# Optimization experiments

Measured on AMD Instinct MI355X. Metric: run time of the kernel, lower is better.

## Reference

```python
import jax, jax.numpy as jnp
import numpy as np
import math, itertools

NUM_FEATURES = 128
NUM_ELEMENTS = 10
BATCH = 2048
LS_IN = [0, 1, 2]            # coupling irreps 0e+1o+2e (parity = (-1)^l)
BLOCKS = [(0, 1), (1, -1)]   # output irreps 0e, 1o as (L, parity)
CORRELATION = 3


def _su2_cg(j1, m1, j2, m2, j3, m3):
    if m3 != m1 + m2 or not (abs(j1 - j2) <= j3 <= j1 + j2):
        return 0.0
    f = math.factorial
    pref = math.sqrt((2 * j3 + 1) * f(j3 + j1 - j2) * f(j3 - j1 + j2) * f(j1 + j2 - j3) / f(j1 + j2 + j3 + 1))
    pref *= math.sqrt(f(j3 + m3) * f(j3 - m3) * f(j1 - m1) * f(j1 + m1) * f(j2 - m2) * f(j2 + m2))
    s = 0.0
    for k in range(max(0, j2 - j3 - m1, j1 - j3 + m2), min(j1 + j2 - j3, j1 - m1, j2 + m2) + 1):
        s += (-1) ** k / (f(k) * f(j1 + j2 - j3 - k) * f(j1 - m1 - k) * f(j2 + m2 - k) * f(j3 - j2 + m1 + k) * f(j3 - j1 - m2 + k))
    return pref * s


def _c2r(l):
    # complex -> real spherical harmonic change of basis (unitary)
    Q = np.zeros((2 * l + 1, 2 * l + 1), dtype=complex)
    Q[l, l] = 1.0
    for m in range(1, l + 1):
        Q[l + m, l + m] = (-1) ** m / math.sqrt(2)
        Q[l + m, l - m] = 1 / math.sqrt(2)
        Q[l - m, l - m] = 1j / math.sqrt(2)
        Q[l - m, l + m] = -1j * (-1) ** m / math.sqrt(2)
    return Q


def _real_cg(l1, l2, l3):
    C = np.zeros((2 * l1 + 1, 2 * l2 + 1, 2 * l3 + 1), dtype=complex)
    for m1 in range(-l1, l1 + 1):
        for m2 in range(-l2, l2 + 1):
            m3 = m1 + m2
            if abs(m3) <= l3:
                C[l1 + m1, l2 + m2, l3 + m3] = _su2_cg(l1, m1, l2, m2, l3, m3)
    T = np.einsum('am,bn,co,mno->abc', _c2r(l1).conj(), _c2r(l2).conj(), _c2r(l3), C)
    if np.abs(T.imag).max() > np.abs(T.real).max():
        T = 1j * T  # tensor is purely real or purely imaginary depending on l1+l2+l3
    return np.ascontiguousarray(T.real)


def _build_paths(segs, num_ell, nu):
    # left-to-right CG coupling of nu copies of the input coupling irreps
    cur = {}
    for l, off in segs:
        T = np.zeros((2 * l + 1, num_ell))
        for m in range(2 * l + 1):
            T[m, off + m] = 1.0
        cur.setdefault((l, (-1) ** l), []).append(T)
    for _ in range(nu - 1):
        nxt = {}
        for (la, pa), ts in cur.items():
            for lb, off in segs:
                for lc in range(abs(la - lb), la + lb + 1):
                    C = _real_cg(la, lb, lc)
                    for T in ts:
                        M = np.einsum('abc,a...->c...b', C, T)
                        new = np.zeros(M.shape[:-1] + (num_ell,))
                        new[..., off:off + 2 * lb + 1] = M
                        nxt.setdefault((lc, pa * (-1) ** lb), []).append(new)
        cur = nxt
    return cur


def _u_matrix(segs, num_ell, nu, L, parity):
    # symmetrized, orthonormalized generalized CG basis: (2L+1, num_ell^nu..., P)
    ts = _build_paths(segs, num_ell, nu).get((L, parity), [])
    dimL = 2 * L + 1
    perms = list(itertools.permutations(range(nu)))
    mats = []
    for T in ts:
        S = sum(np.transpose(T, (0,) + tuple(1 + p for p in perm)) for perm in perms) / len(perms)
        mats.append(S.reshape(-1))
    if not mats:
        return np.zeros((dimL,) + (num_ell,) * nu + (0,))
    _, s, Vh = np.linalg.svd(np.stack(mats), full_matrices=False)
    B = Vh[s > 1e-9 * s[0]]
    return np.moveaxis(B.reshape((-1, dimL) + (num_ell,) * nu), 0, -1)


def setup_inputs() -> dict:
    key = jax.random.key(0)
    kx, ky, kw = jax.random.split(key, 3)
    num_ell = sum(2 * l + 1 for l in LS_IN)  # 9
    segs, off = [], 0
    for l in LS_IN:
        segs.append((l, off))
        off += 2 * l + 1
    x = jax.random.normal(kx, (BATCH, NUM_FEATURES, num_ell), dtype=jnp.float32)
    elem = jax.random.randint(ky, (BATCH,), 0, NUM_ELEMENTS)
    y = jax.nn.one_hot(elem, NUM_ELEMENTS, dtype=jnp.float32)  # one-hot element types
    inp = {"x": x, "y": y}
    for bi, (L, par) in enumerate(BLOCKS):
        Us = {nu: _u_matrix(segs, num_ell, nu, L, par) for nu in range(1, CORRELATION + 1)}
        std = 1.0 / max(sum(U.shape[-1] for U in Us.values()), 1)  # RandomNormal(1/total_params)
        for nu, U in Us.items():
            kw, sub = jax.random.split(kw)
            inp[f"U{nu}_{bi}"] = jnp.asarray(U, dtype=jnp.float32)
            inp[f"W{nu}_{bi}"] = std * jax.random.normal(sub, (NUM_ELEMENTS, U.shape[-1], NUM_FEATURES), dtype=jnp.float32)
    return inp


def _block(x, y, U3, U2, U1, W3, W2, W1):
    # x: (B,C,n), y: (B,E); U_nu: (D, n^nu..., P_nu); W_nu: (E, P_nu, C)
    # degree-3 term: fuse per-element weights and x into the last ell axis of U3
    w3 = jnp.einsum('be,epc->bcp', y, W3)            # (B,C,P3)
    z = x[:, :, :, None] * w3[:, :, None, :]         # (B,C,n,P3)
    out = jnp.einsum('dijkp,bckp->bcdij', U3, z)     # (B,C,D,n,n)
    # degree-2 term added, then contract one more ell axis with x
    c2 = jnp.einsum('dijp,bpc->bcdij', U2, jnp.einsum('be,epc->bpc', y, W2)) + out
    out = jnp.einsum('bcdij,bcj->bcdi', c2, x)
    # degree-1 term added, final contraction
    c1 = jnp.einsum('dip,bpc->bcdi', U1, jnp.einsum('be,epc->bpc', y, W1)) + out
    out = jnp.einsum('bcdi,bci->bcd', c1, x)
    B, C, D = out.shape
    return out.reshape(B, C * D)  # mul_ir (mul-major) layout


def reference(x, y, U1_0, U2_0, U3_0, W1_0, W2_0, W3_0, U1_1, U2_1, U3_1, W1_1, W2_1, W3_1):
    o0 = _block(x, y, U3_0, U2_0, U1_0, W3_0, W2_0, W1_0)  # 128x0e block
    o1 = _block(x, y, U3_1, U2_1, U1_1, W3_1, W2_1, W1_1)  # 128x1o block
    return jnp.concatenate([o0, o1], axis=-1)
```

## Files before the change

kernel.cpp:

```cpp
#include <hip/hip_runtime.h>

#define NELL 9
#define CCH  128
#define DB   3
#define P3A  5
#define P2A  3
#define P1A  1
#define P3B  5
#define P2B  2
#define P1B  1
#define NT3  165
#define NT2  45
#define TTOT (NT3 + NT2 + NELL)
#define CPB  8
#define NCG  (CCH / CPB)
#define CHR  128

#define ACC_FENCE2(A0, A1) asm volatile("" \
    : "+v"(A0.x), "+v"(A0.y), "+v"(A0.z), "+v"(A0.w), \
      "+v"(A1.x), "+v"(A1.y), "+v"(A1.z), "+v"(A1.w) :: "memory")

__device__ __forceinline__ void dec3(int t, int& i, int& j, int& k) {
    i = 0;
    for (;;) { const int cnt = (9 - i) * (10 - i) / 2; if (t < cnt) break; t -= cnt; i++; }
    j = i;
    for (;;) { const int cnt = 9 - j; if (t < cnt) break; t -= cnt; j++; }
    k = j + t;
}
__device__ __forceinline__ void dec2(int t, int& i, int& j) {
    i = 0;
    for (;;) { const int cnt = 9 - i; if (t < cnt) break; t -= cnt; i++; }
    j = i + t;
}


__global__ __launch_bounds__(1024)
void sc_build(const float* __restrict__ y, int B, int E, int MAXCH,
              int* __restrict__ wsi)
{
    __shared__ int cnt[1024];
    __shared__ int off[1024];
    int* chunk_e    = wsi + 4;
    int* chunk_base = wsi + 4 + MAXCH;
    int* chunk_len  = wsi + 4 + 2 * MAXCH;
    int* perm       = wsi + 4 + 3 * MAXCH;

    for (int i = threadIdx.x; i < E; i += blockDim.x) cnt[i] = 0;
    __syncthreads();
    for (int b = threadIdx.x; b < B; b += blockDim.x) {
        int e = 0;
        for (int q = 0; q < E; q++) if (y[(size_t)b * E + q] > 0.5f) e = q;
        atomicAdd(&cnt[e], 1);
    }
    __syncthreads();
    if (threadIdx.x == 0) {
        int s = 0;
        for (int e = 0; e < E; e++) { off[e] = s; s += cnt[e]; }
        int nch = 0;
        for (int e = 0; e < E; e++)
            for (int i = 0; i < cnt[e]; i += CHR) {
                chunk_e[nch]    = e;
                chunk_base[nch] = off[e] + i;
                chunk_len[nch]  = (cnt[e] - i < CHR) ? (cnt[e] - i) : CHR;
                nch++;
            }
        wsi[0] = nch;
    }
    __syncthreads();
    for (int i = threadIdx.x; i < E; i += blockDim.x) cnt[i] = 0;
    __syncthreads();
    for (int b = threadIdx.x; b < B; b += blockDim.x) {
        int e = 0;
        for (int q = 0; q < E; q++) if (y[(size_t)b * E + q] > 0.5f) e = q;
        const int r = atomicAdd(&cnt[e], 1);
        perm[off[e] + r] = b;
    }
}

__global__ __launch_bounds__(512)
void sc_main_f(const float* __restrict__ x, const int* __restrict__ wsi,
               int MAXCH,
               const float* __restrict__ U3a, const float* __restrict__ U2a,
               const float* __restrict__ U1a, const float* __restrict__ U3b,
               const float* __restrict__ U2b, const float* __restrict__ U1b,
               const float* __restrict__ W3a, const float* __restrict__ W2a,
               const float* __restrict__ W1a, const float* __restrict__ W3b,
               const float* __restrict__ W2b, const float* __restrict__ W1b,
               float* __restrict__ out)
{
    __shared__ float4 tile[TTOT][CPB];

    const int chunk = blockIdx.x >> 4;
    const int cgrp  = blockIdx.x & (NCG - 1);
    if (chunk >= wsi[0]) return;

    const int e    = wsi[4 + chunk];
    const int base = wsi[4 + MAXCH + chunk];
    const int len  = wsi[4 + 2 * MAXCH + chunk];
    const int* perm = wsi + 4 + 3 * MAXCH;

    const int wv   = threadIdx.x >> 6;
    const int lane = threadIdx.x & 63;
    const int c    = cgrp * CPB + wv;

    const bool v0 = (lane < len);
    const bool v1 = (lane + 64 < len);
    const int b0 = perm[base + (v0 ? lane : 0)];
    const int b1 = perm[base + (v1 ? lane + 64 : 0)];

    float xv0[NELL], xv1[NELL];
    const float* xp0 = x + ((size_t)b0 * CCH + c) * NELL;
    const float* xp1 = x + ((size_t)b1 * CCH + c) * NELL;
#pragma unroll
    for (int i = 0; i < NELL; i++) { xv0[i] = xp0[i]; xv1[i] = xp1[i]; }

    for (int idx = threadIdx.x; idx < TTOT * CPB; idx += 512) {
        const int t  = idx >> 3;
        const int cl = idx & (CPB - 1);
        const int cc = cgrp * CPB + cl;
        float v[4] = {0.f, 0.f, 0.f, 0.f};
        if (t < NT3) {
            int i, j, k;
            dec3(t, i, j, k);
            const float mult = (i == k) ? 1.f : ((i == j || j == k) ? 3.f : 6.f);
            const int ijk = (i * 9 + j) * 9 + k;
#pragma unroll
            for (int p = 0; p < P3A; p++)
                v[0] += U3a[ijk * P3A + p] * W3a[(e * P3A + p) * CCH + cc];
#pragma unroll
            for (int d = 0; d < DB; d++)
#pragma unroll
                for (int p = 0; p < P3B; p++)
                    v[1 + d] += U3b[(d * 729 + ijk) * P3B + p] * W3b[(e * P3B + p) * CCH + cc];
#pragma unroll
            for (int d = 0; d < 4; d++) v[d] *= mult;
        } else if (t < NT3 + NT2) {
            int i, j;
            dec2(t - NT3, i, j);
            const float mult = (i == j) ? 1.f : 2.f;
            const int ij = i * 9 + j;
#pragma unroll
            for (int p = 0; p < P2A; p++)
                v[0] += U2a[ij * P2A + p] * W2a[(e * P2A + p) * CCH + cc];
#pragma unroll
            for (int d = 0; d < DB; d++)
#pragma unroll
                for (int p = 0; p < P2B; p++)
                    v[1 + d] += U2b[(d * 81 + ij) * P2B + p] * W2b[(e * P2B + p) * CCH + cc];
#pragma unroll
            for (int d = 0; d < 4; d++) v[d] *= mult;
        } else {
            const int i = t - NT3 - NT2;
            v[0] = U1a[i] * W1a[e * CCH + cc];
#pragma unroll
            for (int d = 0; d < DB; d++)
                v[1 + d] = U1b[d * 9 + i] * W1b[e * CCH + cc];
        }
        tile[t][cl] = make_float4(v[0], v[1], v[2], v[3]);
    }
    __syncthreads();

    float4 A0 = make_float4(0.f, 0.f, 0.f, 0.f);
    float4 A1 = make_float4(0.f, 0.f, 0.f, 0.f);
    int t = 0;
#pragma unroll
    for (int i = 0; i < NELL; i++) {
#pragma unroll
        for (int j = i; j < NELL; j++) {
            const float p0 = xv0[i] * xv0[j];
            const float p1 = xv1[i] * xv1[j];
#pragma unroll
            for (int k = j; k < NELL; k++) {
                const float m0 = p0 * xv0[k];
                const float m1 = p1 * xv1[k];
                const float4 w = tile[t][wv];
                t++;
                A0.x = fmaf(w.x, m0, A0.x);
                A0.y = fmaf(w.y, m0, A0.y);
                A0.z = fmaf(w.z, m0, A0.z);
                A0.w = fmaf(w.w, m0, A0.w);
                A1.x = fmaf(w.x, m1, A1.x);
                A1.y = fmaf(w.y, m1, A1.y);
                A1.z = fmaf(w.z, m1, A1.z);
                A1.w = fmaf(w.w, m1, A1.w);
            }
            ACC_FENCE2(A0, A1);
        }
    }
#pragma unroll
    for (int i = 0; i < NELL; i++) {
#pragma unroll
        for (int j = i; j < NELL; j++) {
            const float p0 = xv0[i] * xv0[j];
            const float p1 = xv1[i] * xv1[j];
            const float4 w = tile[t][wv];
            t++;
            A0.x = fmaf(w.x, p0, A0.x);
            A0.y = fmaf(w.y, p0, A0.y);
            A0.z = fmaf(w.z, p0, A0.z);
            A0.w = fmaf(w.w, p0, A0.w);
            A1.x = fmaf(w.x, p1, A1.x);
            A1.y = fmaf(w.y, p1, A1.y);
            A1.z = fmaf(w.z, p1, A1.z);
            A1.w = fmaf(w.w, p1, A1.w);
        }
        ACC_FENCE2(A0, A1);
    }
#pragma unroll
    for (int i = 0; i < NELL; i++) {
        const float4 w = tile[t][wv];
        t++;
        A0.x = fmaf(w.x, xv0[i], A0.x);
        A0.y = fmaf(w.y, xv0[i], A0.y);
        A0.z = fmaf(w.z, xv0[i], A0.z);
        A0.w = fmaf(w.w, xv0[i], A0.w);
        A1.x = fmaf(w.x, xv1[i], A1.x);
        A1.y = fmaf(w.y, xv1[i], A1.y);
        A1.z = fmaf(w.z, xv1[i], A1.z);
        A1.w = fmaf(w.w, xv1[i], A1.w);
    }
    ACC_FENCE2(A0, A1);

    if (v0) {
        float* op = out + (size_t)b0 * (CCH * 4);
        op[c] = A0.x;
        op[CCH + c * DB + 0] = A0.y;
        op[CCH + c * DB + 1] = A0.z;
        op[CCH + c * DB + 2] = A0.w;
    }
    if (v1) {
        float* op = out + (size_t)b1 * (CCH * 4);
        op[c] = A1.x;
        op[CCH + c * DB + 0] = A1.y;
        op[CCH + c * DB + 1] = A1.z;
        op[CCH + c * DB + 2] = A1.w;
    }
}

__global__ __launch_bounds__(CCH)
void sc_direct(const float* __restrict__ x, const float* __restrict__ y, int E,
               const float* __restrict__ U3a, const float* __restrict__ U2a, const float* __restrict__ U1a,
               const float* __restrict__ U3b, const float* __restrict__ U2b, const float* __restrict__ U1b,
               const float* __restrict__ W3a, const float* __restrict__ W2a, const float* __restrict__ W1a,
               const float* __restrict__ W3b, const float* __restrict__ W2b, const float* __restrict__ W1b,
               float* __restrict__ out)
{
    const int c = threadIdx.x;
    const int b = blockIdx.x;

    float xv[NELL];
#pragma unroll
    for (int i = 0; i < NELL; i++) xv[i] = x[(b * CCH + c) * NELL + i];

    int e = 0;
    for (int q = 0; q < E; q++) if (y[b * E + q] > 0.5f) e = q;

    float t3a[P3A] = {}, t3b[DB * P3B] = {};
    float t2a[P2A] = {}, t2b[DB * P2B] = {};
    float t1a = 0.f, t1b[DB] = {};

    for (int i = 0; i < NELL; i++) {
        const float xi = xv[i];
        for (int j = 0; j < NELL; j++) {
            const float xij = xi * xv[j];
            const int ij = i * 9 + j;
#pragma unroll
            for (int p = 0; p < P2A; p++)
                t2a[p] = fmaf(U2a[ij * P2A + p], xij, t2a[p]);
#pragma unroll
            for (int d = 0; d < DB; d++)
#pragma unroll
                for (int p = 0; p < P2B; p++)
                    t2b[d * P2B + p] = fmaf(U2b[(d * 81 + ij) * P2B + p], xij, t2b[d * P2B + p]);
            for (int k = 0; k < NELL; k++) {
                const float m = xij * xv[k];
                const int ijk = ij * 9 + k;
#pragma unroll
                for (int p = 0; p < P3A; p++)
                    t3a[p] = fmaf(U3a[ijk * P3A + p], m, t3a[p]);
#pragma unroll
                for (int d = 0; d < DB; d++)
#pragma unroll
                    for (int p = 0; p < P3B; p++)
                        t3b[d * P3B + p] = fmaf(U3b[(d * 729 + ijk) * P3B + p], m, t3b[d * P3B + p]);
            }
        }
    }
#pragma unroll
    for (int i = 0; i < NELL; i++) {
        t1a = fmaf(U1a[i], xv[i], t1a);
#pragma unroll
        for (int d = 0; d < DB; d++)
            t1b[d] = fmaf(U1b[d * 9 + i], xv[i], t1b[d]);
    }

    float o0 = 0.f;
#pragma unroll
    for (int p = 0; p < P3A; p++) o0 = fmaf(W3a[(e * P3A + p) * CCH + c], t3a[p], o0);
#pragma unroll
    for (int p = 0; p < P2A; p++) o0 = fmaf(W2a[(e * P2A + p) * CCH + c], t2a[p], o0);
    o0 = fmaf(W1a[e * CCH + c], t1a, o0);

    float o1[DB] = {};
#pragma unroll
    for (int p = 0; p < P3B; p++) {
        const float w = W3b[(e * P3B + p) * CCH + c];
#pragma unroll
        for (int d = 0; d < DB; d++) o1[d] = fmaf(w, t3b[d * P3B + p], o1[d]);
    }
#pragma unroll
    for (int p = 0; p < P2B; p++) {
        const float w = W2b[(e * P2B + p) * CCH + c];
#pragma unroll
        for (int d = 0; d < DB; d++) o1[d] = fmaf(w, t2b[d * P2B + p], o1[d]);
    }
    {
        const float w = W1b[e * CCH + c];
#pragma unroll
        for (int d = 0; d < DB; d++) o1[d] = fmaf(w, t1b[d], o1[d]);
    }

    float* op = out + b * (CCH * 4);
    op[c] = o0;
#pragma unroll
    for (int d = 0; d < DB; d++) op[CCH + c * DB + d] = o1[d];
}

extern "C" void kernel_launch(void* const* d_in, const int* in_sizes, int n_in,
                              void* d_out, int out_size, void* d_ws, size_t ws_size,
                              hipStream_t stream)
{
    int ix = 0;
    for (int i = 1; i < n_in; i++)
        if (in_sizes[i] > in_sizes[ix]) ix = i;
    int B = in_sizes[ix] / (CCH * NELL);
    bool ok = (n_in == 14) && (B > 0) && (in_sizes[ix] == B * CCH * NELL);

    int iy = -1, E = 0;
    if (ok) {
        for (int i = 0; i < n_in; i++) {
            if (i == ix) continue;
            if (in_sizes[i] % B == 0) {
                int Ec = in_sizes[i] / B;
                if (Ec >= 2 && Ec <= 1024) {
                    if (iy < 0) { iy = i; E = Ec; } else { ok = false; }
                }
            }
        }
        if (iy < 0) ok = false;
    }

    int iU1a = -1, iU2a = -1, iU3a = -1, iU1b = -1, iU2b = -1, iU3b = -1;
    int iW1a = -1, iW1b = -1, iW2a = -1, iW2b = -1, iW3a = -1, iW3b = -1;
    if (ok) {
        for (int i = 0; i < n_in && ok; i++) {
            if (i == ix || i == iy) continue;
            int s = in_sizes[i];
            if      (s == 9 * P1A)        { if (iU1a < 0) iU1a = i; else ok = false; }
            else if (s == 81 * P2A)       { if (iU2a < 0) iU2a = i; else ok = false; }
            else if (s == 729 * P3A)      { if (iU3a < 0) iU3a = i; else ok = false; }
            else if (s == 27 * P1B)       { if (iU1b < 0) iU1b = i; else ok = false; }
            else if (s == 243 * P2B)      { if (iU2b < 0) iU2b = i; else ok = false; }
            else if (s == 2187 * P3B)     { if (iU3b < 0) iU3b = i; else ok = false; }
            else if (s == E * P1A * CCH)  { if (iW1a < 0) iW1a = i; else if (iW1b < 0) iW1b = i; else ok = false; }
            else if (s == E * P2A * CCH)  { if (iW2a < 0) iW2a = i; else ok = false; }
            else if (s == E * P2B * CCH)  { if (iW2b < 0) iW2b = i; else ok = false; }
            else if (s == E * P3A * CCH)  { if (iW3a < 0) iW3a = i; else if (iW3b < 0) iW3b = i; else ok = false; }
            else ok = false;
        }
        if (iU1a < 0 || iU2a < 0 || iU3a < 0 || iU1b < 0 || iU2b < 0 || iU3b < 0 ||
            iW1a < 0 || iW1b < 0 || iW2a < 0 || iW2b < 0 || iW3a < 0 || iW3b < 0)
            ok = false;
    }

    const int MAXCH = (ok ? B / CHR + E + 1 : 1);
    const size_t int_bytes = (size_t)(4 + 3 * MAXCH + (ok ? B : 1)) * sizeof(int);

    if (ok && ws_size >= int_bytes && B >= 2 && E <= 1024) {
        int* wsi = (int*)d_ws;
        hipLaunchKernelGGL(sc_build, dim3(1), dim3(1024), 0, stream,
                           (const float*)d_in[iy], B, E, MAXCH, wsi);
        hipLaunchKernelGGL(sc_main_f, dim3(MAXCH * NCG), dim3(512), 0, stream,
                           (const float*)d_in[ix], wsi, MAXCH,
                           (const float*)d_in[iU3a], (const float*)d_in[iU2a], (const float*)d_in[iU1a],
                           (const float*)d_in[iU3b], (const float*)d_in[iU2b], (const float*)d_in[iU1b],
                           (const float*)d_in[iW3a], (const float*)d_in[iW2a], (const float*)d_in[iW1a],
                           (const float*)d_in[iW3b], (const float*)d_in[iW2b], (const float*)d_in[iW1b],
                           (float*)d_out);
    } else {
        if (!ok) {
            ix = 0; iy = 1;
            B = in_sizes[0] / (CCH * NELL);
            E = (B > 0) ? in_sizes[1] / B : 1;
            iU1a = 2;  iW1a = 3;  iU2a = 4;  iW2a = 5;  iU3a = 6;  iW3a = 7;
            iU1b = 8;  iW1b = 9;  iU2b = 10; iW2b = 11; iU3b = 12; iW3b = 13;
        }
        hipLaunchKernelGGL(sc_direct, dim3(B), dim3(CCH), 0, stream,
                           (const float*)d_in[ix], (const float*)d_in[iy], E,
                           (const float*)d_in[iU3a], (const float*)d_in[iU2a], (const float*)d_in[iU1a],
                           (const float*)d_in[iU3b], (const float*)d_in[iU2b], (const float*)d_in[iU1b],
                           (const float*)d_in[iW3a], (const float*)d_in[iW2a], (const float*)d_in[iW1a],
                           (const float*)d_in[iW3b], (const float*)d_in[iW2b], (const float*)d_in[iW1b],
                           (float*)d_out);
    }
}
```

Baseline: 32.90 us.

## Process four batch rows per lane with fewer channels per block

Each lane now accumulates four batch rows instead of two, chunks grow to 256 rows, and a block covers only 2 channels with 128 threads, so each shared-memory weight load is reused across more FMAs. The build kernel also caches each row's element index in the workspace instead of rescanning y twice. The changes are meant to cut LDS traffic per FMA and build-kernel work. The cost is more registers per thread, a larger per-block tile build relative to the compute, and less parallelism when chunks are small.

```diff
diff --git a/kernel.cpp b/kernel.cpp
--- a/kernel.cpp
+++ b/kernel.cpp
@@ -12,13 +12,15 @@
 #define NT3  165
 #define NT2  45
 #define TTOT (NT3 + NT2 + NELL)
-#define CPB  8
+#define CPB  2
 #define NCG  (CCH / CPB)
-#define CHR  128
-
-#define ACC_FENCE2(A0, A1) asm volatile("" \
+#define CHR  256
+
+#define ACC_FENCE4(A0, A1, A2, A3) asm volatile("" \
     : "+v"(A0.x), "+v"(A0.y), "+v"(A0.z), "+v"(A0.w), \
-      "+v"(A1.x), "+v"(A1.y), "+v"(A1.z), "+v"(A1.w) :: "memory")
+      "+v"(A1.x), "+v"(A1.y), "+v"(A1.z), "+v"(A1.w), \
+      "+v"(A2.x), "+v"(A2.y), "+v"(A2.z), "+v"(A2.w), \
+      "+v"(A3.x), "+v"(A3.y), "+v"(A3.z), "+v"(A3.w) :: "memory")
 
 __device__ __forceinline__ void dec3(int t, int& i, int& j, int& k) {
     i = 0;
@@ -44,12 +46,14 @@
     int* chunk_base = wsi + 4 + MAXCH;
     int* chunk_len  = wsi + 4 + 2 * MAXCH;
     int* perm       = wsi + 4 + 3 * MAXCH;
+    int* eArr       = wsi + 4 + 3 * MAXCH + B;
 
     for (int i = threadIdx.x; i < E; i += blockDim.x) cnt[i] = 0;
     __syncthreads();
     for (int b = threadIdx.x; b < B; b += blockDim.x) {
         int e = 0;
         for (int q = 0; q < E; q++) if (y[(size_t)b * E + q] > 0.5f) e = q;
+        eArr[b] = e;
         atomicAdd(&cnt[e], 1);
     }
     __syncthreads();
@@ -70,14 +74,13 @@
     for (int i = threadIdx.x; i < E; i += blockDim.x) cnt[i] = 0;
     __syncthreads();
     for (int b = threadIdx.x; b < B; b += blockDim.x) {
-        int e = 0;
-        for (int q = 0; q < E; q++) if (y[(size_t)b * E + q] > 0.5f) e = q;
+        const int e = eArr[b];
         const int r = atomicAdd(&cnt[e], 1);
         perm[off[e] + r] = b;
     }
 }
 
-__global__ __launch_bounds__(512)
+__global__ __launch_bounds__(128)
 void sc_main_f(const float* __restrict__ x, const int* __restrict__ wsi,
                int MAXCH,
                const float* __restrict__ U3a, const float* __restrict__ U2a,
@@ -90,7 +93,7 @@
 {
     __shared__ float4 tile[TTOT][CPB];
 
-    const int chunk = blockIdx.x >> 4;
+    const int chunk = blockIdx.x >> 6;
     const int cgrp  = blockIdx.x & (NCG - 1);
     if (chunk >= wsi[0]) return;
 
@@ -105,17 +108,27 @@
 
     const bool v0 = (lane < len);
     const bool v1 = (lane + 64 < len);
+    const bool v2 = (lane + 128 < len);
+    const bool v3 = (lane + 192 < len);
     const int b0 = perm[base + (v0 ? lane : 0)];
     const int b1 = perm[base + (v1 ? lane + 64 : 0)];
-
-    float xv0[NELL], xv1[NELL];
-    const float* xp0 = x + ((size_t)b0 * CCH + c) * NELL;
-    const float* xp1 = x + ((size_t)b1 * CCH + c) * NELL;
-#pragma unroll
-    for (int i = 0; i < NELL; i++) { xv0[i] = xp0[i]; xv1[i] = xp1[i]; }
-
-    for (int idx = threadIdx.x; idx < TTOT * CPB; idx += 512) {
-        const int t  = idx >> 3;
+    const int b2 = perm[base + (v2 ? lane + 128 : 0)];
+    const int b3 = perm[base + (v3 ? lane + 192 : 0)];
+
+    float xv0[NELL], xv1[NELL], xv2[NELL], xv3[NELL];
+    {
+        const float* xp0 = x + ((size_t)b0 * CCH + c) * NELL;
+        const float* xp1 = x + ((size_t)b1 * CCH + c) * NELL;
+        const float* xp2 = x + ((size_t)b2 * CCH + c) * NELL;
+        const float* xp3 = x + ((size_t)b3 * CCH + c) * NELL;
+#pragma unroll
+        for (int i = 0; i < NELL; i++) {
+            xv0[i] = xp0[i]; xv1[i] = xp1[i]; xv2[i] = xp2[i]; xv3[i] = xp3[i];
+        }
+    }
+
+    for (int idx = threadIdx.x; idx < TTOT * CPB; idx += 128) {
+        const int t  = idx >> 1;
         const int cl = idx & (CPB - 1);
         const int cc = cgrp * CPB + cl;
         float v[4] = {0.f, 0.f, 0.f, 0.f};
@@ -162,6 +175,8 @@
 
     float4 A0 = make_float4(0.f, 0.f, 0.f, 0.f);
     float4 A1 = make_float4(0.f, 0.f, 0.f, 0.f);
+    float4 A2 = make_float4(0.f, 0.f, 0.f, 0.f);
+    float4 A3 = make_float4(0.f, 0.f, 0.f, 0.f);
     int t = 0;
 #pragma unroll
     for (int i = 0; i < NELL; i++) {
@@ -169,10 +184,14 @@
         for (int j = i; j < NELL; j++) {
             const float p0 = xv0[i] * xv0[j];
             const float p1 = xv1[i] * xv1[j];
+            const float p2 = xv2[i] * xv2[j];
+            const float p3 = xv3[i] * xv3[j];
 #pragma unroll
             for (int k = j; k < NELL; k++) {
                 const float m0 = p0 * xv0[k];
                 const float m1 = p1 * xv1[k];
+                const float m2 = p2 * xv2[k];
+                const float m3 = p3 * xv3[k];
                 const float4 w = tile[t][wv];
                 t++;
                 A0.x = fmaf(w.x, m0, A0.x);
@@ -183,8 +202,16 @@
                 A1.y = fmaf(w.y, m1, A1.y);
                 A1.z = fmaf(w.z, m1, A1.z);
                 A1.w = fmaf(w.w, m1, A1.w);
+                A2.x = fmaf(w.x, m2, A2.x);
+                A2.y = fmaf(w.y, m2, A2.y);
+                A2.z = fmaf(w.z, m2, A2.z);
+                A2.w = fmaf(w.w, m2, A2.w);
+                A3.x = fmaf(w.x, m3, A3.x);
+                A3.y = fmaf(w.y, m3, A3.y);
+                A3.z = fmaf(w.z, m3, A3.z);
+                A3.w = fmaf(w.w, m3, A3.w);
             }
-            ACC_FENCE2(A0, A1);
+            ACC_FENCE4(A0, A1, A2, A3);
         }
     }
 #pragma unroll
@@ -193,6 +220,8 @@
         for (int j = i; j < NELL; j++) {
             const float p0 = xv0[i] * xv0[j];
             const float p1 = xv1[i] * xv1[j];
+            const float p2 = xv2[i] * xv2[j];
+            const float p3 = xv3[i] * xv3[j];
             const float4 w = tile[t][wv];
             t++;
             A0.x = fmaf(w.x, p0, A0.x);
@@ -203,8 +232,16 @@
             A1.y = fmaf(w.y, p1, A1.y);
             A1.z = fmaf(w.z, p1, A1.z);
             A1.w = fmaf(w.w, p1, A1.w);
-        }
-        ACC_FENCE2(A0, A1);
+            A2.x = fmaf(w.x, p2, A2.x);
+            A2.y = fmaf(w.y, p2, A2.y);
+            A2.z = fmaf(w.z, p2, A2.z);
+            A2.w = fmaf(w.w, p2, A2.w);
+            A3.x = fmaf(w.x, p3, A3.x);
+            A3.y = fmaf(w.y, p3, A3.y);
+            A3.z = fmaf(w.z, p3, A3.z);
+            A3.w = fmaf(w.w, p3, A3.w);
+        }
+        ACC_FENCE4(A0, A1, A2, A3);
     }
 #pragma unroll
     for (int i = 0; i < NELL; i++) {
@@ -218,8 +255,16 @@
         A1.y = fmaf(w.y, xv1[i], A1.y);
         A1.z = fmaf(w.z, xv1[i], A1.z);
         A1.w = fmaf(w.w, xv1[i], A1.w);
-    }
-    ACC_FENCE2(A0, A1);
+        A2.x = fmaf(w.x, xv2[i], A2.x);
+        A2.y = fmaf(w.y, xv2[i], A2.y);
+        A2.z = fmaf(w.z, xv2[i], A2.z);
+        A2.w = fmaf(w.w, xv2[i], A2.w);
+        A3.x = fmaf(w.x, xv3[i], A3.x);
+        A3.y = fmaf(w.y, xv3[i], A3.y);
+        A3.z = fmaf(w.z, xv3[i], A3.z);
+        A3.w = fmaf(w.w, xv3[i], A3.w);
+    }
+    ACC_FENCE4(A0, A1, A2, A3);
 
     if (v0) {
         float* op = out + (size_t)b0 * (CCH * 4);
@@ -234,6 +279,20 @@
         op[CCH + c * DB + 0] = A1.y;
         op[CCH + c * DB + 1] = A1.z;
         op[CCH + c * DB + 2] = A1.w;
+    }
+    if (v2) {
+        float* op = out + (size_t)b2 * (CCH * 4);
+        op[c] = A2.x;
+        op[CCH + c * DB + 0] = A2.y;
+        op[CCH + c * DB + 1] = A2.z;
+        op[CCH + c * DB + 2] = A2.w;
+    }
+    if (v3) {
+        float* op = out + (size_t)b3 * (CCH * 4);
+        op[c] = A3.x;
+        op[CCH + c * DB + 0] = A3.y;
+        op[CCH + c * DB + 1] = A3.z;
+        op[CCH + c * DB + 2] = A3.w;
     }
 }
 
@@ -374,13 +433,13 @@
     }
 
     const int MAXCH = (ok ? B / CHR + E + 1 : 1);
-    const size_t int_bytes = (size_t)(4 + 3 * MAXCH + (ok ? B : 1)) * sizeof(int);
+    const size_t int_bytes = (size_t)(4 + 3 * MAXCH + 2 * (ok ? B : 1)) * sizeof(int);
 
     if (ok && ws_size >= int_bytes && B >= 2 && E <= 1024) {
         int* wsi = (int*)d_ws;
         hipLaunchKernelGGL(sc_build, dim3(1), dim3(1024), 0, stream,
                            (const float*)d_in[iy], B, E, MAXCH, wsi);
-        hipLaunchKernelGGL(sc_main_f, dim3(MAXCH * NCG), dim3(512), 0, stream,
+        hipLaunchKernelGGL(sc_main_f, dim3(MAXCH * NCG), dim3(128), 0, stream,
                            (const float*)d_in[ix], wsi, MAXCH,
                            (const float*)d_in[iU3a], (const float*)d_in[iU2a], (const float*)d_in[iU1a],
                            (const float*)d_in[iU3b], (const float*)d_in[iU2b], (const float*)d_in[iU1b],
```

New measurement: 35.50 us. 1.08x slower.
